# Kernel optimization log

Measured on AMD Instinct MI355X. Metric: run time of the kernel, lower is better.

The kernel has to match this reference:

```python
import jax, jax.numpy as jnp
import numpy as np
from functools import partial

D = 1024
H = 4 * D
E = 8
K_TOP = 2
B, T = 4, 2048
NEG_INF = jnp.float32(-1e30)


def setup_inputs() -> dict:
    key = jax.random.key(0)
    ks = jax.random.split(key, 12)
    s = 0.02
    return {
        "x": jax.random.normal(ks[0], (B, T, D), jnp.float32),
        "noise": jax.random.normal(ks[1], (B, T, E), jnp.float32),
        "gate_w": jax.random.normal(ks[2], (E, D), jnp.float32) * s,
        "gate_b": jnp.zeros((E,), jnp.float32),
        "var_w": jax.random.normal(ks[3], (E, D), jnp.float32) * s,
        "var_b": jnp.zeros((E,), jnp.float32),
        "w1": jax.random.normal(ks[4], (E, H, D), jnp.float32) * s,
        "b1": jnp.zeros((E, H), jnp.float32),
        "w2": jax.random.normal(ks[5], (E, D, H), jnp.float32) * s,
        "b2": jnp.zeros((E, D), jnp.float32),
    }


def reference(x, noise, gate_w, gate_b, var_w, var_b, w1, b1, w2, b2):
    # Noisy top-k gating
    logits = jnp.einsum("btd,ed->bte", x, gate_w) + gate_b          # [B,T,E]
    std = jax.nn.softplus(jnp.einsum("btd,ed->bte", x, var_w) + var_b)
    noisy = logits + noise * std                                      # [B,T,E]
    _, idx = jax.lax.top_k(noisy, K_TOP)                              # [B,T,K]
    # boolean top-k mask over experts
    mask = (idx[..., None] == jnp.arange(E)).any(axis=-2)             # [B,T,E]
    coef = jax.nn.softmax(jnp.where(mask, noisy, NEG_INF), axis=-1)   # zeros outside top-k

    # Combine: sum_e coef_e * FFN_e(x). coef is exactly 0 for non-selected
    # experts, so this equals the masked gather/scatter math. Scan over the
    # small expert dim to avoid a [E,B,T,H] intermediate.
    coef_e = jnp.moveaxis(coef, -1, 0)                                # [E,B,T]

    def body(acc, ew):
        w1e, b1e, w2e, b2e, ce = ew
        h = jax.nn.relu(jnp.einsum("btd,hd->bth", x, w1e) + b1e)
        y = jnp.einsum("bth,dh->btd", h, w2e) + b2e
        return acc + y * ce[..., None], None

    out, _ = jax.lax.scan(body, jnp.zeros_like(x), (w1, b1, w2, b2, coef_e))
    return out
```

## Files before the change

kernel.cpp:

```cpp
#include <hip/hip_runtime.h>
#include <hip/hip_bf16.h>
#include <math.h>

#define NTOK 8192
#define DD   1024
#define HH   4096
#define NE   8
#define BM 256
#define BN 256
#define SLOT_CAP (2 * NTOK + NE * BM)

typedef __bf16 bf16;
typedef __bf16 bf16x8 __attribute__((ext_vector_type(8)));
typedef __bf16 bf16x4 __attribute__((ext_vector_type(4)));
typedef float  f32x4  __attribute__((ext_vector_type(4)));

typedef __attribute__((address_space(3))) unsigned char lds_u8;
typedef const __attribute__((address_space(1))) unsigned char g_u8;

__device__ __forceinline__ void gload16(const bf16* g, bf16* l) {
  __builtin_amdgcn_global_load_lds((g_u8*)g, (lds_u8*)l, 16, 0, 0);
}

__device__ __forceinline__ float softplus_f(float v) {
  return fmaxf(v, 0.f) + log1pf(expf(-fabsf(v)));
}

__global__ __launch_bounds__(64) void moe_gate_kernel(
    const float* __restrict__ x, const float* __restrict__ noise,
    const float* __restrict__ gate_w, const float* __restrict__ gate_b,
    const float* __restrict__ var_w,  const float* __restrict__ var_b,
    float* __restrict__ coef2, int* __restrict__ t2e, int* __restrict__ counts)
{
  const int t = blockIdx.x;
  const int lane = threadIdx.x;
  const float* xt = x + (size_t)t * DD;
  float pg[NE], pv[NE];
  #pragma unroll
  for (int e = 0; e < NE; ++e) { pg[e] = 0.f; pv[e] = 0.f; }
  #pragma unroll 4
  for (int i = 0; i < DD / 64; ++i) {
    const int d = lane + i * 64;
    const float xv = xt[d];
    #pragma unroll
    for (int e = 0; e < NE; ++e) {
      pg[e] = fmaf(xv, gate_w[e * DD + d], pg[e]);
      pv[e] = fmaf(xv, var_w[e * DD + d], pv[e]);
    }
  }
  #pragma unroll
  for (int e = 0; e < NE; ++e) {
    #pragma unroll
    for (int off = 32; off; off >>= 1) {
      pg[e] += __shfl_xor(pg[e], off);
      pv[e] += __shfl_xor(pv[e], off);
    }
  }
  if (lane == 0) {
    float noisy[NE];
    #pragma unroll
    for (int e = 0; e < NE; ++e) {
      const float lg = pg[e] + gate_b[e];
      const float sd = softplus_f(pv[e] + var_b[e]);
      noisy[e] = lg + noise[t * NE + e] * sd;
    }
    int i1 = 0; float n1 = noisy[0];
    #pragma unroll
    for (int e = 1; e < NE; ++e) if (noisy[e] > n1) { n1 = noisy[e]; i1 = e; }
    int i2 = -1; float n2 = -3.0e38f;
    #pragma unroll
    for (int e = 0; e < NE; ++e) if (e != i1 && noisy[e] > n2) { n2 = noisy[e]; i2 = e; }
    const float e2 = expf(n2 - n1);
    const float den = 1.f + e2;
    coef2[t * 2 + 0] = 1.f / den;
    coef2[t * 2 + 1] = e2 / den;
    t2e[t * 2 + 0] = i1;
    t2e[t * 2 + 1] = i2;
    atomicAdd(&counts[i1], 1);
    atomicAdd(&counts[i2], 1);
  }
}

__global__ void moe_offsets_kernel(const int* __restrict__ counts, int* __restrict__ po) {
  if (threadIdx.x == 0) {
    int acc = 0;
    po[0] = 0;
    for (int e = 0; e < NE; ++e) {
      acc += ((counts[e] + BM - 1) / BM) * BM;
      po[e + 1] = acc;
    }
  }
}

__global__ __launch_bounds__(256) void moe_scatter_kernel(
    const int* __restrict__ t2e, const float* __restrict__ coef2,
    const int* __restrict__ po, int* __restrict__ cnt2,
    int* __restrict__ assign_tok, float* __restrict__ slot_coef)
{
  const int t = blockIdx.x * 256 + threadIdx.x;
  if (t >= NTOK) return;
  #pragma unroll
  for (int k = 0; k < 2; ++k) {
    const int e = t2e[t * 2 + k];
    const int pos = atomicAdd(&cnt2[e], 1);
    const int slot = po[e] + pos;
    assign_tok[slot] = t;
    slot_coef[slot] = coef2[t * 2 + k];
  }
}

__global__ __launch_bounds__(256) void cvt_bf16_kernel(const float* __restrict__ src,
                                                       bf16* __restrict__ dst, int n4) {
  for (int i = blockIdx.x * 256 + threadIdx.x; i < n4; i += gridDim.x * 256) {
    const float4 f = ((const float4*)src)[i];
    bf16x4 v;
    v[0] = (bf16)f.x; v[1] = (bf16)f.y; v[2] = (bf16)f.z; v[3] = (bf16)f.w;
    ((bf16x4*)dst)[i] = v;
  }
}

template<int KDIM, int KSTRIDE, int NCOLS, bool FFN1>
__global__ __launch_bounds__(512, 2) void moe_gemm8_kernel(
    const bf16* __restrict__ Asrc, const bf16* __restrict__ Wsrc,
    const float* __restrict__ bias,
    const int* __restrict__ assign_tok, const float* __restrict__ slot_coef,
    const int* __restrict__ po,
    bf16* __restrict__ hout, float* __restrict__ out,
    int chunk_base, int gx)
{
  constexpr int NI  = KDIM / 128;
  constexpr int KHT = KDIM / 32;
  __shared__ bf16 smA[32768];
  __shared__ bf16 smB[32768];
  __shared__ int toks[BM];

  const int nwg = gx * (NCOLS / BN);
  const int lin = blockIdx.x;
  const int q = nwg >> 3, r = nwg & 7;
  const int xcd = lin & 7, idx = lin >> 3;
  const int wg = (xcd < r ? xcd * (q + 1) : r * (q + 1) + (xcd - r) * q) + idx;
  const int bx = wg % gx, by = wg / gx;

  const int row0 = chunk_base + bx * BM;
  const int po8 = po[NE];
  if (row0 >= po8) return;
  int e = 0;
  while (row0 >= po[e + 1]) ++e;
  const int bn0 = by * BN;
  const size_t kbase = (size_t)blockIdx.z * KDIM;
  const bf16* We = Wsrc + (size_t)e * ((size_t)HH * DD) + kbase;
  const bf16* As = Asrc + kbase;

  const int tid = threadIdx.x, lane = tid & 63, wid = tid >> 6;
  if (tid < BM) toks[tid] = assign_tok[row0 + tid];
  __syncthreads();

  const int srcc = (((lane & 3) ^ ((lane >> 2) & 3)) * 8);
  const int rt0 = wid * 16 + (lane >> 2);
  const int rt1 = (8 + wid) * 16 + (lane >> 2);
  int ar0, ar1;
  if constexpr (FFN1) {
    const int s0 = toks[rt0]; ar0 = s0 < 0 ? 0 : s0;
    const int s1 = toks[rt1]; ar1 = s1 < 0 ? 0 : s1;
  } else {
    ar0 = row0 - chunk_base + rt0;
    ar1 = row0 - chunk_base + rt1;
  }
  const bf16* ap0 = As + (size_t)ar0 * KSTRIDE + srcc;
  const bf16* ap1 = As + (size_t)ar1 * KSTRIDE + srcc;
  const bf16* bp0 = We + (size_t)(bn0 + rt0) * KSTRIDE + srcc;
  const bf16* bp1 = We + (size_t)(bn0 + rt1) * KSTRIDE + srcc;

  auto stage = [&](int rr, int kh) {
    const int ko = kh * 32;
    gload16(ap0 + ko, &smA[rr * 8192 + wid * 512]);
    gload16(ap1 + ko, &smA[rr * 8192 + (8 + wid) * 512]);
    gload16(bp0 + ko, &smB[rr * 8192 + wid * 512]);
    gload16(bp1 + ko, &smB[rr * 8192 + (8 + wid) * 512]);
  };

  const int wr = wid >> 2, wc = wid & 3;
  const int la = lane & 15, hi = lane >> 4;
  const int cph = (hi ^ (la & 3)) * 8;
  const int aBase = wr * 4096 + la * 32 + cph;
  const int bBase = wc * 2048 + la * 32 + cph;

  f32x4 acc[8][4];
  #pragma unroll
  for (int m = 0; m < 8; ++m)
    #pragma unroll
    for (int n = 0; n < 4; ++n) acc[m][n] = {0.f, 0.f, 0.f, 0.f};

  stage(0, 0); stage(1, 1); stage(2, 2);

  for (int i = 0; i < NI; ++i) {
    #pragma unroll
    for (int pp = 0; pp < 4; ++pp) {
      asm volatile("s_waitcnt vmcnt(8)" ::: "memory");
      asm volatile("s_barrier" ::: "memory");
      bf16x8 a0[4], bb[4];
      #pragma unroll
      for (int m = 0; m < 4; ++m)
        a0[m] = *(const bf16x8*)(&smA[pp * 8192 + aBase + m * 512]);
      #pragma unroll
      for (int n = 0; n < 4; ++n)
        bb[n] = *(const bf16x8*)(&smB[pp * 8192 + bBase + n * 512]);
      stage((pp + 3) & 3, (i * 4 + 3 + pp) & (KHT - 1));
      __builtin_amdgcn_s_setprio(1);
      #pragma unroll
      for (int m = 0; m < 4; ++m)
        #pragma unroll
        for (int n = 0; n < 4; ++n)
          acc[m][n] = __builtin_amdgcn_mfma_f32_16x16x32_bf16(a0[m], bb[n], acc[m][n], 0, 0, 0);
      __builtin_amdgcn_s_setprio(0);
      bf16x8 a1[4];
      #pragma unroll
      for (int m = 0; m < 4; ++m)
        a1[m] = *(const bf16x8*)(&smA[pp * 8192 + aBase + (4 + m) * 512]);
      __builtin_amdgcn_s_setprio(1);
      #pragma unroll
      for (int m = 0; m < 4; ++m)
        #pragma unroll
        for (int n = 0; n < 4; ++n)
          acc[4 + m][n] = __builtin_amdgcn_mfma_f32_16x16x32_bf16(a1[m], bb[n], acc[4 + m][n], 0, 0, 0);
      __builtin_amdgcn_s_setprio(0);
    }
  }

  if constexpr (FFN1) {
    const int hrow0 = row0 - chunk_base;
    #pragma unroll
    for (int n = 0; n < 4; ++n) {
      const int col = bn0 + wc * 64 + n * 16 + la;
      const float bb = bias[e * NCOLS + col];
      #pragma unroll
      for (int m = 0; m < 8; ++m) {
        const int rl = wr * 128 + m * 16 + hi * 4;
        #pragma unroll
        for (int rr = 0; rr < 4; ++rr) {
          float v = acc[m][n][rr] + bb;
          v = v > 0.f ? v : 0.f;
          hout[(size_t)(hrow0 + rl + rr) * HH + col] = (bf16)v;
        }
      }
    }
  } else {
    const bool addb = (blockIdx.z == 0);
    #pragma unroll
    for (int n = 0; n < 4; ++n) {
      const int col = bn0 + wc * 64 + n * 16 + la;
      const float bb = addb ? bias[e * NCOLS + col] : 0.f;
      #pragma unroll
      for (int m = 0; m < 8; ++m) {
        const int rl = wr * 128 + m * 16 + hi * 4;
        #pragma unroll
        for (int rr = 0; rr < 4; ++rr) {
          const int tl = rl + rr;
          const int tok = toks[tl];
          if (tok >= 0) {
            const float c = slot_coef[row0 + tl];
            atomicAdd(out + (size_t)tok * DD + col, c * (acc[m][n][rr] + bb));
          }
        }
      }
    }
  }
}

extern "C" void kernel_launch(void* const* d_in, const int* in_sizes, int n_in,
                              void* d_out, int out_size, void* d_ws, size_t ws_size,
                              hipStream_t stream) {
  const float* x      = (const float*)d_in[0];
  const float* noise  = (const float*)d_in[1];
  const float* gate_w = (const float*)d_in[2];
  const float* gate_b = (const float*)d_in[3];
  const float* var_w  = (const float*)d_in[4];
  const float* var_b  = (const float*)d_in[5];
  const float* w1     = (const float*)d_in[6];
  const float* b1     = (const float*)d_in[7];
  const float* w2     = (const float*)d_in[8];
  const float* b2     = (const float*)d_in[9];
  float* out = (float*)d_out;
  (void)in_sizes; (void)n_in; (void)out_size;

  char* ws = (char*)d_ws;
  size_t off = 0;
  auto alloc = [&](size_t bytes) {
    off = (off + 255) & ~(size_t)255;
    size_t o = off;
    off += bytes;
    return o;
  };
  bf16*  xb         = (bf16*)(ws + alloc((size_t)NTOK * DD * 2));
  float* coef2      = (float*)(ws + alloc((size_t)NTOK * 2 * 4));
  int*   t2e        = (int*)(ws + alloc((size_t)NTOK * 2 * 4));
  int*   counts     = (int*)(ws + alloc(64));
  int*   cnt2       = counts + 8;
  int*   po         = (int*)(ws + alloc(64));
  int*   assign_tok = (int*)(ws + alloc((size_t)SLOT_CAP * 4));
  float* slot_coef  = (float*)(ws + alloc((size_t)SLOT_CAP * 4));
  bf16*  w1b        = (bf16*)(ws + alloc((size_t)NE * HH * DD * 2));
  bf16*  w2b        = (bf16*)(ws + alloc((size_t)NE * DD * HH * 2));
  off = (off + 255) & ~(size_t)255;
  const size_t h_avail = ws_size > off ? ws_size - off : 0;
  int chunk_rows = (int)(h_avail / ((size_t)HH * 2));
  chunk_rows = (chunk_rows / BM) * BM;
  if (chunk_rows < BM) chunk_rows = BM;
  if (chunk_rows > SLOT_CAP) chunk_rows = SLOT_CAP;
  bf16* hbuf = (bf16*)(ws + off);

  hipMemsetAsync(counts, 0, 64, stream);
  hipMemsetAsync(assign_tok, 0xFF, (size_t)SLOT_CAP * 4, stream);
  hipMemsetAsync(out, 0, (size_t)NTOK * DD * 4, stream);

  moe_gate_kernel<<<NTOK, 64, 0, stream>>>(x, noise, gate_w, gate_b, var_w, var_b,
                                           coef2, t2e, counts);
  moe_offsets_kernel<<<1, 64, 0, stream>>>(counts, po);
  moe_scatter_kernel<<<NTOK / 256, 256, 0, stream>>>(t2e, coef2, po, cnt2,
                                                     assign_tok, slot_coef);
  cvt_bf16_kernel<<<2048, 256, 0, stream>>>(x, xb, NTOK * DD / 4);
  cvt_bf16_kernel<<<2048, 256, 0, stream>>>(w1, w1b, NE * HH * DD / 4);
  cvt_bf16_kernel<<<2048, 256, 0, stream>>>(w2, w2b, NE * DD * HH / 4);

  const int rounds = (SLOT_CAP + chunk_rows - 1) / chunk_rows;
  for (int r = 0; r < rounds; ++r) {
    const int cb = r * chunk_rows;
    const int rows_here = (cb + chunk_rows <= SLOT_CAP) ? chunk_rows : (SLOT_CAP - cb);
    const int gx = rows_here / BM;
    dim3 g1(gx * (HH / BN), 1, 1);
    moe_gemm8_kernel<DD, DD, HH, true><<<g1, 512, 0, stream>>>(
        xb, w1b, b1, assign_tok, slot_coef, po, hbuf, nullptr, cb, gx);
    dim3 g2(gx * (DD / BN), 1, 2);
    moe_gemm8_kernel<HH / 2, HH, DD, false><<<g2, 512, 0, stream>>>(
        hbuf, w2b, b2, assign_tok, slot_coef, po, nullptr, out, cb, gx);
  }
}
```

Measured before the change: 952.5 us.

## Restructure MoE GEMM mainloop to double-buffered 64-wide K tiles with 8x8 swizzle

Replaces the 4-stage ring of 32-wide K slices with a two-buffer pipeline of 64-wide K tiles, using a new XOR swizzle and an interleaved LDS-read/MFMA schedule split into four barrier-separated phases. The FFN2 split-K factor rises from 2 to 4, which adds workgroups for the smaller second GEMM at the cost of more atomic accumulation into the output. The intent is fewer barriers per unit of K and better overlap of LDS reads with MFMAs. The risk is that waiting on vmcnt(0) each tile exposes global latency that the deeper prefetch used to hide.

```diff
diff --git a/kernel.cpp b/kernel.cpp
--- a/kernel.cpp
+++ b/kernel.cpp
@@ -119,8 +119,31 @@
   }
 }
 
+#define MFMA16(AR, BR, MB)                                                   \
+  __builtin_amdgcn_s_setprio(1);                                             \
+  _Pragma("unroll")                                                          \
+  for (int m_ = 0; m_ < 4; ++m_)                                             \
+    _Pragma("unroll")                                                        \
+    for (int n_ = 0; n_ < 4; ++n_)                                           \
+      acc[MB + m_][n_] = __builtin_amdgcn_mfma_f32_16x16x32_bf16(            \
+          AR[m_], BR[n_], acc[MB + m_][n_], 0, 0, 0);                        \
+  __builtin_amdgcn_s_setprio(0);
+
+#define RD_A(DST, MOFF, SZ)                                                  \
+  _Pragma("unroll")                                                          \
+  for (int m_ = 0; m_ < 4; ++m_)                                             \
+    DST[m_] = *(const bf16x8*)(Ab + aBase + (MOFF + m_) * 1024 + SZ);
+
+#define RD_B(DST, SZ)                                                        \
+  _Pragma("unroll")                                                          \
+  for (int n_ = 0; n_ < 4; ++n_)                                             \
+    DST[n_] = *(const bf16x8*)(Bb + bBase + n_ * 1024 + SZ);
+
+#define VMCNT0 asm volatile("s_waitcnt vmcnt(0)" ::: "memory")
+#define BAR    asm volatile("s_barrier" ::: "memory")
+
 template<int KDIM, int KSTRIDE, int NCOLS, bool FFN1>
-__global__ __launch_bounds__(512, 2) void moe_gemm8_kernel(
+__global__ __launch_bounds__(512, 2) void moe_gemm_kernel(
     const bf16* __restrict__ Asrc, const bf16* __restrict__ Wsrc,
     const float* __restrict__ bias,
     const int* __restrict__ assign_tok, const float* __restrict__ slot_coef,
@@ -128,13 +151,12 @@
     bf16* __restrict__ hout, float* __restrict__ out,
     int chunk_base, int gx)
 {
-  constexpr int NI  = KDIM / 128;
-  constexpr int KHT = KDIM / 32;
-  __shared__ bf16 smA[32768];
-  __shared__ bf16 smB[32768];
+  constexpr int NK = KDIM / 64;
+  __shared__ bf16 smA[2 * BM * 64];
+  __shared__ bf16 smB[2 * BN * 64];
   __shared__ int toks[BM];
 
-  const int nwg = gx * (NCOLS / BN);
+  const int nwg = gridDim.x;
   const int lin = blockIdx.x;
   const int q = nwg >> 3, r = nwg & 7;
   const int xcd = lin & 7, idx = lin >> 3;
@@ -155,35 +177,45 @@
   if (tid < BM) toks[tid] = assign_tok[row0 + tid];
   __syncthreads();
 
-  const int srcc = (((lane & 3) ^ ((lane >> 2) & 3)) * 8);
-  const int rt0 = wid * 16 + (lane >> 2);
-  const int rt1 = (8 + wid) * 16 + (lane >> 2);
-  int ar0, ar1;
-  if constexpr (FFN1) {
-    const int s0 = toks[rt0]; ar0 = s0 < 0 ? 0 : s0;
-    const int s1 = toks[rt1]; ar1 = s1 < 0 ? 0 : s1;
-  } else {
-    ar0 = row0 - chunk_base + rt0;
-    ar1 = row0 - chunk_base + rt1;
-  }
-  const bf16* ap0 = As + (size_t)ar0 * KSTRIDE + srcc;
-  const bf16* ap1 = As + (size_t)ar1 * KSTRIDE + srcc;
-  const bf16* bp0 = We + (size_t)(bn0 + rt0) * KSTRIDE + srcc;
-  const bf16* bp1 = We + (size_t)(bn0 + rt1) * KSTRIDE + srcc;
-
-  auto stage = [&](int rr, int kh) {
-    const int ko = kh * 32;
-    gload16(ap0 + ko, &smA[rr * 8192 + wid * 512]);
-    gload16(ap1 + ko, &smA[rr * 8192 + (8 + wid) * 512]);
-    gload16(bp0 + ko, &smB[rr * 8192 + wid * 512]);
-    gload16(bp1 + ko, &smB[rr * 8192 + (8 + wid) * 512]);
+  const int srcc = ((tid & 7) ^ ((tid >> 3) & 7)) * 8;
+  const bf16* ap[2][2];
+  const bf16* bp[2][2];
+  #pragma unroll
+  for (int h = 0; h < 2; ++h)
+    #pragma unroll
+    for (int j = 0; j < 2; ++j) {
+      const int row = h * 128 + j * 64 + (tid >> 3);
+      int ar;
+      if constexpr (FFN1) {
+        const int s = toks[row];
+        ar = s < 0 ? 0 : s;
+      } else {
+        ar = row0 - chunk_base + row;
+      }
+      ap[h][j] = As + (size_t)ar * KSTRIDE + srcc;
+      bp[h][j] = We + (size_t)(bn0 + row) * KSTRIDE + srcc;
+    }
+
+  auto stageAll = [&](int b, int kt) {
+    const int ko = kt * 64;
+    #pragma unroll
+    for (int h = 0; h < 2; ++h)
+      #pragma unroll
+      for (int j = 0; j < 2; ++j)
+        gload16(ap[h][j] + ko, &smA[b * 16384 + h * 8192 + (j * 512 + tid) * 8]);
+    #pragma unroll
+    for (int h = 0; h < 2; ++h)
+      #pragma unroll
+      for (int j = 0; j < 2; ++j)
+        gload16(bp[h][j] + ko, &smB[b * 16384 + h * 8192 + (j * 512 + tid) * 8]);
   };
 
   const int wr = wid >> 2, wc = wid & 3;
   const int la = lane & 15, hi = lane >> 4;
-  const int cph = (hi ^ (la & 3)) * 8;
-  const int aBase = wr * 4096 + la * 32 + cph;
-  const int bBase = wc * 2048 + la * 32 + cph;
+  const int aBase = (wr * 128 + la) * 64;
+  const int bBase = (wc * 64 + la) * 64;
+  const int sz0 = ((hi)     ^ (la & 7)) * 8;
+  const int sz1 = ((4 + hi) ^ (la & 7)) * 8;
 
   f32x4 acc[8][4];
   #pragma unroll
@@ -191,40 +223,37 @@
     #pragma unroll
     for (int n = 0; n < 4; ++n) acc[m][n] = {0.f, 0.f, 0.f, 0.f};
 
-  stage(0, 0); stage(1, 1); stage(2, 2);
-
-  for (int i = 0; i < NI; ++i) {
-    #pragma unroll
-    for (int pp = 0; pp < 4; ++pp) {
-      asm volatile("s_waitcnt vmcnt(8)" ::: "memory");
-      asm volatile("s_barrier" ::: "memory");
-      bf16x8 a0[4], bb[4];
-      #pragma unroll
-      for (int m = 0; m < 4; ++m)
-        a0[m] = *(const bf16x8*)(&smA[pp * 8192 + aBase + m * 512]);
-      #pragma unroll
-      for (int n = 0; n < 4; ++n)
-        bb[n] = *(const bf16x8*)(&smB[pp * 8192 + bBase + n * 512]);
-      stage((pp + 3) & 3, (i * 4 + 3 + pp) & (KHT - 1));
-      __builtin_amdgcn_s_setprio(1);
-      #pragma unroll
-      for (int m = 0; m < 4; ++m)
-        #pragma unroll
-        for (int n = 0; n < 4; ++n)
-          acc[m][n] = __builtin_amdgcn_mfma_f32_16x16x32_bf16(a0[m], bb[n], acc[m][n], 0, 0, 0);
-      __builtin_amdgcn_s_setprio(0);
-      bf16x8 a1[4];
-      #pragma unroll
-      for (int m = 0; m < 4; ++m)
-        a1[m] = *(const bf16x8*)(&smA[pp * 8192 + aBase + (4 + m) * 512]);
-      __builtin_amdgcn_s_setprio(1);
-      #pragma unroll
-      for (int m = 0; m < 4; ++m)
-        #pragma unroll
-        for (int n = 0; n < 4; ++n)
-          acc[4 + m][n] = __builtin_amdgcn_mfma_f32_16x16x32_bf16(a1[m], bb[n], acc[4 + m][n], 0, 0, 0);
-      __builtin_amdgcn_s_setprio(0);
-    }
+  stageAll(0, 0);
+
+  bf16x8 aX[4], aY[4], bb0[4], bb1[4];
+  for (int kt = 0; kt < NK; ++kt) {
+    const int b = kt & 1, nb = b ^ 1;
+    const bf16* Ab = smA + b * 16384;
+    const bf16* Bb = smB + b * 16384;
+
+    VMCNT0;
+    BAR;
+    RD_A(aX, 0, sz0);
+    RD_B(bb0, sz0);
+    RD_A(aY, 0, sz1);
+    if (kt + 1 < NK) stageAll(nb, kt + 1);
+    MFMA16(aX, bb0, 0);
+    BAR;
+
+    BAR;
+    RD_B(bb1, sz1);
+    RD_A(aX, 4, sz1);
+    MFMA16(aY, bb1, 0);
+    BAR;
+
+    BAR;
+    RD_A(aY, 4, sz0);
+    MFMA16(aX, bb1, 4);
+    BAR;
+
+    BAR;
+    MFMA16(aY, bb0, 4);
+    BAR;
   }
 
   if constexpr (FFN1) {
@@ -328,10 +357,10 @@
     const int rows_here = (cb + chunk_rows <= SLOT_CAP) ? chunk_rows : (SLOT_CAP - cb);
     const int gx = rows_here / BM;
     dim3 g1(gx * (HH / BN), 1, 1);
-    moe_gemm8_kernel<DD, DD, HH, true><<<g1, 512, 0, stream>>>(
+    moe_gemm_kernel<DD, DD, HH, true><<<g1, 512, 0, stream>>>(
         xb, w1b, b1, assign_tok, slot_coef, po, hbuf, nullptr, cb, gx);
-    dim3 g2(gx * (DD / BN), 1, 2);
-    moe_gemm8_kernel<HH / 2, HH, DD, false><<<g2, 512, 0, stream>>>(
+    dim3 g2(gx * (DD / BN), 1, 4);
+    moe_gemm_kernel<HH / 4, HH, DD, false><<<g2, 512, 0, stream>>>(
         hbuf, w2b, b2, assign_tok, slot_coef, po, nullptr, out, cb, gx);
   }
 }
```

Result: slower. 1.065 ms (+11.8%).
